# Kernel optimization log

Measured on AMD Instinct MI355X. Metric: run time of the kernel, lower is better.

## Reference

```python
import jax, jax.numpy as jnp
import numpy as np

B, C, M, H, W = 4, 12, 2, 320, 320
TOL = 1e-6
MAX_ITER = 10


def to_c(t):
    # [..., 2] real -> complex
    return jax.lax.complex(t[..., 0], t[..., 1])


def to_r(t):
    return jnp.stack([jnp.real(t), jnp.imag(t)], axis=-1)


def fft2c(x):
    return jnp.fft.fft2(x, axes=(-2, -1), norm='ortho')


def ifft2c(x):
    return jnp.fft.ifft2(x, axes=(-2, -1), norm='ortho')


def A_op(x, sm, mk):
    # x: [B,M,H,W] complex, sm: [B,C,M,H,W] complex, mk: [B,C,H,W] real
    coil_imgs = jnp.sum(x[:, None] * sm, axis=2)  # [B,C,H,W]
    return fft2c(coil_imgs) * mk


def AT_op(y, sm, mk):
    img = ifft2c(y * mk)  # [B,C,H,W]
    return jnp.sum(jnp.conj(sm) * img[:, :, None], axis=1)  # [B,M,H,W]


def cg_solve(x0, Mop, tol=TOL, max_iter=MAX_ITER):
    b = x0.shape[0]
    x0x0 = jnp.sum(jnp.abs(x0.reshape(b, -1)) ** 2, axis=-1)  # [B] real

    def body(carry, _):
        x, r, p, rr = carry
        active = jnp.min(rr / x0x0) > tol  # tol check, gated like the while-loop
        q = Mop(p)
        pq = jnp.sum((p * jnp.conj(q)).reshape(b, -1), axis=-1)  # complexDot(p, q)
        alpha = rr.astype(x0.dtype) / pq  # complex_div(rr, <p,q>)
        a = alpha[:, None, None, None]
        x_new = x + a * p
        r_new = r - a * q
        rr_new = jnp.sum(jnp.abs(r_new.reshape(b, -1)) ** 2, axis=-1)
        beta = (rr_new / rr)[:, None, None, None].astype(x0.dtype)
        p_new = r_new + beta * p
        new = (x_new, r_new, p_new, rr_new)
        carry = jax.tree.map(lambda n, o: jnp.where(active, n, o), new, carry)
        return carry, None

    rr0 = jnp.sum(jnp.abs(x0.reshape(b, -1)) ** 2, axis=-1)
    init = (jnp.zeros_like(x0), x0, x0, rr0)
    (x, _, _, _), _ = jax.lax.scan(body, init, None, length=max_iter)
    return x


def setup_inputs() -> dict:
    key = jax.random.key(0)
    k1, k2, k3, k4 = jax.random.split(key, 4)
    x = jax.random.normal(k1, (B, M, H, W, 2), dtype=jnp.float32)
    y = jax.random.normal(k2, (B, C, H, W, 2), dtype=jnp.float32)
    smaps = jax.random.normal(k3, (B, C, M, H, W, 2), dtype=jnp.float32) * 0.2
    mask = jax.random.randint(k4, (B, C, H, W, 1), 0, 2).astype(jnp.float32)
    lambda_a = jnp.full((1,), 0.05, dtype=jnp.float32)
    return {"x": x, "y": y, "smaps": smaps, "mask": mask, "lambda_a": lambda_a}


def reference(x, y, smaps, mask, lambda_a):
    z = to_c(x)          # [B,M,H,W]
    yc = to_c(y)         # [B,C,H,W]
    sm = to_c(smaps)     # [B,C,M,H,W]
    mk = mask[..., 0]    # [B,C,H,W]
    lam = lambda_a[0]

    x0 = lam * AT_op(yc, sm, mk) + z

    def Mop(p):
        return lam * AT_op(A_op(p, sm, mk), sm, mk) + p

    return to_r(cg_solve(x0, Mop))
```

## Files before the change

### kernel.cpp

```cpp
#include <hip/hip_runtime.h>
#include <math.h>

#define NB 4
#define NC 12
#define NM 2
#define NN 320
#define NHW (NN*NN)
#define NBC (NB*NC)
#define CG_TOL 1e-6f
#define NITER 10
#define PBLK 400
#define QBLK 320
#define QROW 4
#define LSTR (NN + 2)

#define TWO_PI_F 6.28318530717958647692f

typedef float2 c32;

__device__ __forceinline__ c32 cmul(c32 a, c32 b){ return make_float2(a.x*b.x - a.y*b.y, a.x*b.y + a.y*b.x); }
__device__ __forceinline__ c32 cmulj(c32 a, c32 b){ return make_float2(a.x*b.x + a.y*b.y, a.x*b.y - a.y*b.x); }
__device__ __forceinline__ c32 cadd(c32 a, c32 b){ return make_float2(a.x+b.x, a.y+b.y); }
__device__ __forceinline__ c32 csub(c32 a, c32 b){ return make_float2(a.x-b.x, a.y-b.y); }
__device__ __forceinline__ c32 cscale(c32 a, float s){ return make_float2(a.x*s, a.y*s); }

template<bool CONJ>
__device__ __forceinline__ c32 twmul(c32 a, c32 t){
  return CONJ ? make_float2(a.x*t.x + a.y*t.y, a.y*t.x - a.x*t.y)
              : make_float2(a.x*t.x - a.y*t.y, a.y*t.x + a.x*t.y);
}

__device__ __forceinline__ float wave_reduce_f(float v) {
  #pragma unroll
  for (int off = 32; off >= 1; off >>= 1) v += __shfl_xor(v, off, 64);
  return v;
}
__device__ __forceinline__ c32 wave_reduce_c(c32 v) {
  #pragma unroll
  for (int off = 32; off >= 1; off >>= 1) {
    v.x += __shfl_xor(v.x, off, 64);
    v.y += __shfl_xor(v.y, off, 64);
  }
  return v;
}

__global__ __launch_bounds__(256)
void twiddle_init(c32* __restrict__ T320, c32* __restrict__ T64)
{
  const int t = threadIdx.x;
  {
    float s, c; sincosf(TWO_PI_F * (float)t / 320.f, &s, &c);
    T320[t] = make_float2(c, s);
  }
  if (t < 32) {
    float s, c; sincosf(TWO_PI_F * (float)t / 64.f, &s, &c);
    T64[t] = make_float2(c, s);
  }
}

template<bool FWD>
__device__ __forceinline__ void radix5(c32 V[5]) {
  constexpr float C1 = 0.30901699437494745f;
  constexpr float S1 = 0.9510565162951535f;
  constexpr float C2 = -0.8090169943749475f;
  constexpr float S2 = 0.5877852522924731f;
  constexpr float sg = FWD ? -1.f : 1.f;
  const c32 w1 = make_float2(C1,  sg*S1);
  const c32 w2 = make_float2(C2,  sg*S2);
  const c32 w3 = make_float2(C2, -sg*S2);
  const c32 w4 = make_float2(C1, -sg*S1);
  c32 v0=V[0], v1=V[1], v2=V[2], v3=V[3], v4=V[4];
  V[0] = cadd(cadd(v0, v1), cadd(cadd(v2, v3), v4));
  V[1] = cadd(v0, cadd(cadd(cmul(v1,w1), cmul(v2,w2)), cadd(cmul(v3,w3), cmul(v4,w4))));
  V[2] = cadd(v0, cadd(cadd(cmul(v1,w2), cmul(v2,w4)), cadd(cmul(v3,w1), cmul(v4,w3))));
  V[3] = cadd(v0, cadd(cadd(cmul(v1,w3), cmul(v2,w1)), cadd(cmul(v3,w4), cmul(v4,w2))));
  V[4] = cadd(v0, cadd(cadd(cmul(v1,w4), cmul(v2,w3)), cadd(cmul(v3,w2), cmul(v4,w1))));
}

template<bool FWD>
__device__ __forceinline__ void fft320_x2(c32 A[5], c32 B[5],
                                          const c32 ct[4], const c32 tw[6], int lane)
{
  radix5<FWD>(A);
  radix5<FWD>(B);
  #pragma unroll
  for (int k = 1; k < 5; ++k) {
    A[k] = twmul<FWD>(A[k], ct[k-1]);
    B[k] = twmul<FWD>(B[k], ct[k-1]);
  }
  #pragma unroll
  for (int s = 0; s < 6; ++s) {
    const int m = 32 >> s;
    const c32 w = tw[s];
    const bool up = (lane & m) != 0;
    c32 oA[5], oB[5];
    #pragma unroll
    for (int k = 0; k < 5; ++k) { oA[k].x = __shfl_xor(A[k].x, m, 64); oA[k].y = __shfl_xor(A[k].y, m, 64); }
    #pragma unroll
    for (int k = 0; k < 5; ++k) { oB[k].x = __shfl_xor(B[k].x, m, 64); oB[k].y = __shfl_xor(B[k].y, m, 64); }
    #pragma unroll
    for (int k = 0; k < 5; ++k) {
      c32 loA = cadd(A[k], oA[k]);
      c32 hiA = twmul<FWD>(csub(oA[k], A[k]), w);
      A[k] = up ? hiA : loA;
      c32 loB = cadd(B[k], oB[k]);
      c32 hiB = twmul<FWD>(csub(oB[k], B[k]), w);
      B[k] = up ? hiB : loB;
    }
  }
}

template<bool FWD>
__device__ __forceinline__ void fft320_one(c32 A[5], const c32 ct[4], const c32 tw[6], int lane)
{
  radix5<FWD>(A);
  #pragma unroll
  for (int k = 1; k < 5; ++k) A[k] = twmul<FWD>(A[k], ct[k-1]);
  #pragma unroll
  for (int s = 0; s < 6; ++s) {
    const int m = 32 >> s;
    const c32 w = tw[s];
    const bool up = (lane & m) != 0;
    c32 o[5];
    #pragma unroll
    for (int k = 0; k < 5; ++k) { o[k].x = __shfl_xor(A[k].x, m, 64); o[k].y = __shfl_xor(A[k].y, m, 64); }
    #pragma unroll
    for (int k = 0; k < 5; ++k) {
      c32 lo = cadd(A[k], o[k]);
      c32 hi = twmul<FWD>(csub(o[k], A[k]), w);
      A[k] = up ? hi : lo;
    }
  }
}

#define LOAD_TWIDDLES \
  c32 ct[4], tw[6]; \
  _Pragma("unroll") for (int k_ = 0; k_ < 4; ++k_) ct[k_] = T320[(k_ + 1) * lane]; \
  _Pragma("unroll") for (int s_ = 0; s_ < 6; ++s_) tw[s_] = T64[(lane & ((32 >> s_) - 1)) << s_];

template<bool FWD, bool MASK_IN>
__global__ __launch_bounds__(256)
void fft_pass(const c32* __restrict__ in, c32* __restrict__ out,
              const float* __restrict__ mask,
              const c32* __restrict__ T320, const c32* __restrict__ T64)
{
  __shared__ c32 tile[8][LSTR];
  const int tid = threadIdx.x, lane = tid & 63, wv = tid >> 6;
  const int bc = blockIdx.y, r0 = blockIdx.x * 8;
  LOAD_TWIDDLES
  const int rv6 = __brev((unsigned)lane) >> 26;
  const int rA = r0 + wv*2, rB = rA + 1;
  c32 A[5], B[5];
  #pragma unroll
  for (int j = 0; j < 5; ++j) {
    const size_t iA = ((size_t)bc * NN + rA) * NN + lane + 64*j;
    const size_t iB = ((size_t)bc * NN + rB) * NN + lane + 64*j;
    A[j] = in[iA]; B[j] = in[iB];
    if constexpr (MASK_IN) { A[j] = cscale(A[j], mask[iA]); B[j] = cscale(B[j], mask[iB]); }
  }
  fft320_x2<FWD>(A, B, ct, tw, lane);
  #pragma unroll
  for (int k = 0; k < 5; ++k) {
    tile[wv*2    ][k + 5*rv6] = A[k];
    tile[wv*2 + 1][k + 5*rv6] = B[k];
  }
  __syncthreads();
  #pragma unroll
  for (int it = 0; it < 10; ++it) {
    const int idx = it * 256 + tid, u = idx >> 3, d = idx & 7;
    out[((size_t)bc * NN + u) * NN + (r0 + d)] = tile[d][u];
  }
}

__global__ __launch_bounds__(256)
void init_combine(const c32* __restrict__ img, const c32* __restrict__ smaps,
                  const c32* __restrict__ z, c32* __restrict__ x,
                  c32* __restrict__ r, c32* __restrict__ p,
                  const float* __restrict__ lam, float* __restrict__ part)
{
  const int b  = blockIdx.y;
  const int hw = blockIdx.x * 256 + threadIdx.x;
  const float l0 = lam[0] * (1.f / (float)NN);
  c32 a0 = make_float2(0.f,0.f), a1 = make_float2(0.f,0.f);
  #pragma unroll
  for (int c = 0; c < NC; ++c) {
    c32 iv = img[(size_t)(b*NC + c) * NHW + hw];
    c32 s0 = smaps[(size_t)((b*NC + c)*NM + 0) * NHW + hw];
    c32 s1 = smaps[(size_t)((b*NC + c)*NM + 1) * NHW + hw];
    a0 = cadd(a0, cmulj(s0, iv));
    a1 = cadd(a1, cmulj(s1, iv));
  }
  const size_t i0 = (size_t)(b*NM + 0) * NHW + hw;
  const size_t i1 = (size_t)(b*NM + 1) * NHW + hw;
  c32 x00 = cadd(cscale(a0, l0), z[i0]);
  c32 x01 = cadd(cscale(a1, l0), z[i1]);
  x[i0] = make_float2(0.f,0.f); x[i1] = make_float2(0.f,0.f);
  r[i0] = x00; r[i1] = x01;
  p[i0] = x00; p[i1] = x01;
  float acc = x00.x*x00.x + x00.y*x00.y + x01.x*x01.x + x01.y*x01.y;
  acc = wave_reduce_f(acc);
  __shared__ float sred[4];
  const int lane = threadIdx.x & 63, wv = threadIdx.x >> 6;
  if (lane == 0) sred[wv] = acc;
  __syncthreads();
  if (threadIdx.x == 0) part[b*PBLK + blockIdx.x] = sred[0]+sred[1]+sred[2]+sred[3];
}

__global__ __launch_bounds__(256)
void fft_comb(c32* __restrict__ out, const c32* __restrict__ pin,
              const c32* __restrict__ rres, c32* __restrict__ pout,
              const c32* __restrict__ smaps,
              float* __restrict__ rr, float* __restrict__ flags,
              const float* __restrict__ part1, const int it,
              const c32* __restrict__ T320, const c32* __restrict__ T64)
{
  __shared__ c32 tile[8][LSTR];
  __shared__ float sstat[NB];
  const int tid = threadIdx.x, lane = tid & 63, wv = tid >> 6;
  const int bc = blockIdx.y, r0 = blockIdx.x * 8;
  const int b = bc / NC, c = bc - b * NC;
  {
    float s = 0.f;
    for (int j = lane; j < PBLK; j += 64) s += part1[wv*PBLK + j];
    s = wave_reduce_f(s);
    if (lane == 0) sstat[wv] = s;
  }
  __syncthreads();
  float flag;
  if (it == 0) flag = 1.f;
  else {
    float mn = 1e30f;
    #pragma unroll
    for (int bb = 0; bb < NB; ++bb) mn = fminf(mn, sstat[bb] / rr[bb]);
    flag = (mn > CG_TOL) ? 1.f : 0.f;
  }
  if (tid < NB) rr[it*NB + tid] = sstat[tid];
  if (tid == 0) flags[it] = flag;
  if (it != 0 && flag == 0.f) return;
  const float beta = (it != 0) ? sstat[b] / rr[(it-1)*NB + b] : 0.f;
  const bool upd = (it != 0);

  LOAD_TWIDDLES
  const int rv6 = __brev((unsigned)lane) >> 26;
  const int rA = r0 + wv*2, rB = rA + 1;
  const size_t m0 = (size_t)(b*NM + 0) * NHW, m1 = (size_t)(b*NM + 1) * NHW;
  const size_t s0o = (size_t)((b*NC + c)*NM + 0) * NHW, s1o = (size_t)((b*NC + c)*NM + 1) * NHW;
  c32 A[5], B[5];
  #pragma unroll
  for (int j = 0; j < 5; ++j) {
    const size_t hA = (size_t)rA * NN + lane + 64*j;
    const size_t hB = (size_t)rB * NN + lane + 64*j;
    c32 r0A = rres[m0 + hA], r1A = rres[m1 + hA];
    c32 r0B = rres[m0 + hB], r1B = rres[m1 + hB];
    c32 p0A, p1A, p0B, p1B;
    if (upd) {
      p0A = cadd(r0A, cscale(pin[m0 + hA], beta));
      p1A = cadd(r1A, cscale(pin[m1 + hA], beta));
      p0B = cadd(r0B, cscale(pin[m0 + hB], beta));
      p1B = cadd(r1B, cscale(pin[m1 + hB], beta));
      if (c == 0) {
        pout[m0 + hA] = p0A; pout[m1 + hA] = p1A;
        pout[m0 + hB] = p0B; pout[m1 + hB] = p1B;
      }
    } else {
      p0A = r0A; p1A = r1A; p0B = r0B; p1B = r1B;
    }
    A[j] = cadd(cmul(p0A, smaps[s0o + hA]), cmul(p1A, smaps[s1o + hA]));
    B[j] = cadd(cmul(p0B, smaps[s0o + hB]), cmul(p1B, smaps[s1o + hB]));
  }
  fft320_x2<true>(A, B, ct, tw, lane);
  #pragma unroll
  for (int k = 0; k < 5; ++k) {
    tile[wv*2    ][k + 5*rv6] = A[k];
    tile[wv*2 + 1][k + 5*rv6] = B[k];
  }
  __syncthreads();
  #pragma unroll
  for (int it5 = 0; it5 < 10; ++it5) {
    const int idx = it5 * 256 + tid, u = idx >> 3, d = idx & 7;
    out[((size_t)bc * NN + u) * NN + (r0 + d)] = tile[d][u];
  }
}

__global__ __launch_bounds__(256)
void fft_mask_ifft(const c32* __restrict__ in, c32* __restrict__ out,
                   const float* __restrict__ mask, const float* __restrict__ flag,
                   const c32* __restrict__ T320, const c32* __restrict__ T64)
{
  if (flag[0] == 0.f) return;
  __shared__ c32 tile[8][LSTR];
  const int tid = threadIdx.x, lane = tid & 63, wv = tid >> 6;
  const int bc = blockIdx.y, r0 = blockIdx.x * 8;
  LOAD_TWIDDLES
  const int rv6 = __brev((unsigned)lane) >> 26;
  const int rA = r0 + wv*2, rB = rA + 1;
  c32 A[5], B[5];
  #pragma unroll
  for (int j = 0; j < 5; ++j) {
    A[j] = in[((size_t)bc * NN + rA) * NN + lane + 64*j];
    B[j] = in[((size_t)bc * NN + rB) * NN + lane + 64*j];
  }
  fft320_x2<true>(A, B, ct, tw, lane);
  #pragma unroll
  for (int k = 0; k < 5; ++k) {
    const int kh = k + 5*rv6;
    A[k] = cscale(A[k], mask[(size_t)bc * NHW + (size_t)kh * NN + rA]);
    B[k] = cscale(B[k], mask[(size_t)bc * NHW + (size_t)kh * NN + rB]);
  }
  #pragma unroll
  for (int k = 0; k < 5; ++k) {
    tile[wv*2    ][k + 5*rv6] = A[k];
    tile[wv*2 + 1][k + 5*rv6] = B[k];
  }
  #pragma unroll
  for (int j = 0; j < 5; ++j) {
    A[j] = tile[wv*2    ][lane + 64*j];
    B[j] = tile[wv*2 + 1][lane + 64*j];
  }
  fft320_x2<false>(A, B, ct, tw, lane);
  #pragma unroll
  for (int k = 0; k < 5; ++k) {
    tile[wv*2    ][k + 5*rv6] = A[k];
    tile[wv*2 + 1][k + 5*rv6] = B[k];
  }
  __syncthreads();
  #pragma unroll
  for (int it = 0; it < 10; ++it) {
    const int idx = it * 256 + tid, u = idx >> 3, d = idx & 7;
    out[((size_t)bc * NN + u) * NN + (r0 + d)] = tile[d][u];
  }
}

__global__ __launch_bounds__(256)
void ifft_q(const c32* __restrict__ bufin, const c32* __restrict__ smaps,
            const c32* __restrict__ p, c32* __restrict__ q,
            const float* __restrict__ lam, const float* __restrict__ flag,
            c32* __restrict__ pqpart,
            const c32* __restrict__ T320, const c32* __restrict__ T64)
{
  if (flag[0] == 0.f) return;
  __shared__ c32 tile[QROW][LSTR];
  const int tid = threadIdx.x, lane = tid & 63, wv = tid >> 6;
  const int b = blockIdx.y, h = blockIdx.x;
  LOAD_TWIDDLES
  const int rv6 = __brev((unsigned)lane) >> 26;
  const float lq = lam[0] * (1.f / (float)NHW);
  const size_t rowoff = (size_t)h * NN + lane;
  c32 acc0[5], acc1[5];
  #pragma unroll
  for (int j = 0; j < 5; ++j) { acc0[j] = make_float2(0.f,0.f); acc1[j] = make_float2(0.f,0.f); }

  for (int cc = 0; cc < 3; ++cc) {
    const int c = wv * 3 + cc;
    const size_t ib  = (size_t)(b*NC + c) * NHW + rowoff;
    const size_t is0 = (size_t)((b*NC + c)*NM + 0) * NHW + rowoff;
    const size_t is1 = (size_t)((b*NC + c)*NM + 1) * NHW + rowoff;
    c32 A[5], S0[5], S1[5];
    #pragma unroll
    for (int j = 0; j < 5; ++j) {
      A[j] = bufin[ib + 64*j]; S0[j] = smaps[is0 + 64*j]; S1[j] = smaps[is1 + 64*j];
    }
    fft320_one<false>(A, ct, tw, lane);
    #pragma unroll
    for (int k = 0; k < 5; ++k) tile[wv][k + 5*rv6] = A[k];
    #pragma unroll
    for (int j = 0; j < 5; ++j) {
      c32 v = tile[wv][lane + 64*j];
      acc0[j] = cadd(acc0[j], cmulj(S0[j], v));
      acc1[j] = cadd(acc1[j], cmulj(S1[j], v));
    }
  }
  c32* red = &tile[0][0];
  __syncthreads();
  if (wv >= 2) {
    const int base = (wv - 2) * 640;
    #pragma unroll
    for (int j = 0; j < 5; ++j) {
      red[base + j*64 + lane] = acc0[j];
      red[base + 320 + j*64 + lane] = acc1[j];
    }
  }
  __syncthreads();
  if (wv < 2) {
    const int base = wv * 640;
    #pragma unroll
    for (int j = 0; j < 5; ++j) {
      acc0[j] = cadd(acc0[j], red[base + j*64 + lane]);
      acc1[j] = cadd(acc1[j], red[base + 320 + j*64 + lane]);
    }
  }
  __syncthreads();
  if (wv == 1) {
    #pragma unroll
    for (int j = 0; j < 5; ++j) {
      red[j*64 + lane] = acc0[j];
      red[320 + j*64 + lane] = acc1[j];
    }
  }
  __syncthreads();
  if (wv == 0) {
    const size_t i0 = (size_t)(b*NM + 0) * NHW + rowoff;
    const size_t i1 = (size_t)(b*NM + 1) * NHW + rowoff;
    c32 pqs = make_float2(0.f, 0.f);
    #pragma unroll
    for (int j = 0; j < 5; ++j) {
      acc0[j] = cadd(acc0[j], red[j*64 + lane]);
      acc1[j] = cadd(acc1[j], red[320 + j*64 + lane]);
      c32 p0 = p[i0 + 64*j], p1 = p[i1 + 64*j];
      c32 q0 = cadd(cscale(acc0[j], lq), p0);
      c32 q1 = cadd(cscale(acc1[j], lq), p1);
      q[i0 + 64*j] = q0; q[i1 + 64*j] = q1;
      pqs = cadd(pqs, cadd(cmulj(q0, p0), cmulj(q1, p1)));
    }
    pqs = wave_reduce_c(pqs);
    if (lane == 0) pqpart[b*QBLK + h] = pqs;
  }
}

__global__ __launch_bounds__(256)
void update1(c32* __restrict__ x, c32* __restrict__ r,
             const c32* __restrict__ p, const c32* __restrict__ q,
             const float* __restrict__ rr, const c32* __restrict__ pqpart,
             const float* __restrict__ flag, float* __restrict__ part,
             const int it)
{
  if (flag[0] == 0.f) return;
  const int b = blockIdx.y;
  const int t = threadIdx.x;
  c32 s = make_float2(0.f, 0.f);
  for (int j = t; j < QBLK; j += 256) s = cadd(s, pqpart[b*QBLK + j]);
  s = wave_reduce_c(s);
  __shared__ c32 spq[4];
  const int lane = t & 63, wv = t >> 6;
  if (lane == 0) spq[wv] = s;
  __syncthreads();
  const c32 pqv = cadd(cadd(spq[0], spq[1]), cadd(spq[2], spq[3]));
  const float rrv = rr[it*NB + b];
  const float den = pqv.x*pqv.x + pqv.y*pqv.y;
  const c32 alpha = make_float2(rrv * pqv.x / den, -rrv * pqv.y / den);
  const int hw = blockIdx.x * 256 + t;
  float acc = 0.f;
  #pragma unroll
  for (int m = 0; m < NM; ++m) {
    const size_t idx = (size_t)(b*NM + m) * NHW + hw;
    c32 pe = p[idx], qe = q[idx];
    c32 xe = cadd(x[idx], cmul(alpha, pe));
    c32 re = csub(r[idx], cmul(alpha, qe));
    x[idx] = xe; r[idx] = re;
    acc += re.x*re.x + re.y*re.y;
  }
  acc = wave_reduce_f(acc);
  __shared__ float sred[4];
  if (lane == 0) sred[wv] = acc;
  __syncthreads();
  if (t == 0) part[b*PBLK + blockIdx.x] = sred[0]+sred[1]+sred[2]+sred[3];
}

extern "C" void kernel_launch(void* const* d_in, const int* in_sizes, int n_in,
                              void* d_out, int out_size, void* d_ws, size_t ws_size,
                              hipStream_t stream)
{
  const c32*  z   = (const c32*)d_in[0];
  const c32*  y   = (const c32*)d_in[1];
  const c32*  sm  = (const c32*)d_in[2];
  const float* mk = (const float*)d_in[3];
  const float* lam= (const float*)d_in[4];
  c32* x = (c32*)d_out;

  char* base = (char*)d_ws;
  size_t off = 0;
  auto walloc = [&](size_t bytes) -> void* {
    void* ptr = base + off;
    off += (bytes + 255) & ~(size_t)255;
    return ptr;
  };
  c32* buf1   = (c32*)walloc((size_t)NBC * NHW * sizeof(c32));
  c32* buf2   = (c32*)walloc((size_t)NBC * NHW * sizeof(c32));
  c32* rv     = (c32*)walloc((size_t)NB * NM * NHW * sizeof(c32));
  c32* pvA    = (c32*)walloc((size_t)NB * NM * NHW * sizeof(c32));
  c32* pvB    = (c32*)walloc((size_t)NB * NM * NHW * sizeof(c32));
  c32* qv     = (c32*)walloc((size_t)NB * NM * NHW * sizeof(c32));
  c32* pqpart = (c32*)walloc((size_t)NB * QBLK * sizeof(c32));
  float* rr   = (float*)walloc((NITER + 1) * NB * sizeof(float));
  float* flags= (float*)walloc((NITER + 1) * sizeof(float));
  float* part1= (float*)walloc((size_t)NB * PBLK * sizeof(float));
  c32* T320   = (c32*)walloc(256 * sizeof(c32));
  c32* T64    = (c32*)walloc(32 * sizeof(c32));
  (void)ws_size; (void)in_sizes; (void)n_in; (void)out_size;

  dim3 blk256(256);
  dim3 fgrid(NN / 8, NBC);
  dim3 qgrid(QBLK, NB);
  dim3 ugrid(PBLK, NB);

  twiddle_init<<<1, blk256, 0, stream>>>(T320, T64);

  fft_pass<false, true ><<<fgrid, blk256, 0, stream>>>(y,    buf2, mk,      T320, T64);
  fft_pass<false, false><<<fgrid, blk256, 0, stream>>>(buf2, buf1, nullptr, T320, T64);
  init_combine<<<ugrid, blk256, 0, stream>>>(buf1, sm, z, x, rv, pvA, lam, part1);

  for (int i = 0; i < NITER; ++i) {
    c32* pin  = (i & 1) ? pvA : pvB;
    c32* pout = (i & 1) ? pvB : pvA;
    fft_comb<<<fgrid, blk256, 0, stream>>>(buf2, pin, rv, pout, sm, rr, flags, part1, i, T320, T64);
    fft_mask_ifft<<<fgrid, blk256, 0, stream>>>(buf2, buf1, mk, flags + i, T320, T64);
    ifft_q<<<qgrid, blk256, 0, stream>>>(buf1, sm, pout, qv, lam, flags + i, pqpart, T320, T64);
    update1<<<ugrid, blk256, 0, stream>>>(x, rv, pout, qv, rr, pqpart, flags + i, part1, i);
  }
}
```

Baseline: 377.3 us.

## Split LDS tiles into planar real/imag arrays, swap FFT grid order, early-exit CG

Replaces the interleaved complex shared-memory tiles with separate real and imaginary float arrays padded to 328. The goal is to cut LDS bank conflicts in the bit-reversed stores and the transposed reads. The FFT grid now puts batch-coil on blockIdx.x and row groups on blockIdx.y, which changes how blocks are scheduled and how writes are spread across cache and memory channels. fft_comb also returns early once the previous iteration's flag is zero, skipping the partial-sum reduction after convergence, though with ten iterations and the test tolerance this path may rarely trigger.

```diff
diff --git a/kernel.cpp b/kernel.cpp
--- a/kernel.cpp
+++ b/kernel.cpp
@@ -11,8 +11,7 @@
 #define NITER 10
 #define PBLK 400
 #define QBLK 320
-#define QROW 4
-#define LSTR (NN + 2)
+#define LSTRF 328
 
 #define TWO_PI_F 6.28318530717958647692f
 
@@ -144,9 +143,9 @@
               const float* __restrict__ mask,
               const c32* __restrict__ T320, const c32* __restrict__ T64)
 {
-  __shared__ c32 tile[8][LSTR];
+  __shared__ float tX[8][LSTRF], tY[8][LSTRF];
   const int tid = threadIdx.x, lane = tid & 63, wv = tid >> 6;
-  const int bc = blockIdx.y, r0 = blockIdx.x * 8;
+  const int bc = blockIdx.x, r0 = blockIdx.y * 8;
   LOAD_TWIDDLES
   const int rv6 = __brev((unsigned)lane) >> 26;
   const int rA = r0 + wv*2, rB = rA + 1;
@@ -161,14 +160,15 @@
   fft320_x2<FWD>(A, B, ct, tw, lane);
   #pragma unroll
   for (int k = 0; k < 5; ++k) {
-    tile[wv*2    ][k + 5*rv6] = A[k];
-    tile[wv*2 + 1][k + 5*rv6] = B[k];
+    const int i = k + 5*rv6;
+    tX[wv*2    ][i] = A[k].x; tY[wv*2    ][i] = A[k].y;
+    tX[wv*2 + 1][i] = B[k].x; tY[wv*2 + 1][i] = B[k].y;
   }
   __syncthreads();
   #pragma unroll
   for (int it = 0; it < 10; ++it) {
     const int idx = it * 256 + tid, u = idx >> 3, d = idx & 7;
-    out[((size_t)bc * NN + u) * NN + (r0 + d)] = tile[d][u];
+    out[((size_t)bc * NN + u) * NN + (r0 + d)] = make_float2(tX[d][u], tY[d][u]);
   }
 }
 
@@ -214,11 +214,15 @@
               const float* __restrict__ part1, const int it,
               const c32* __restrict__ T320, const c32* __restrict__ T64)
 {
-  __shared__ c32 tile[8][LSTR];
+  __shared__ float tX[8][LSTRF], tY[8][LSTRF];
   __shared__ float sstat[NB];
   const int tid = threadIdx.x, lane = tid & 63, wv = tid >> 6;
-  const int bc = blockIdx.y, r0 = blockIdx.x * 8;
+  const int bc = blockIdx.x, r0 = blockIdx.y * 8;
   const int b = bc / NC, c = bc - b * NC;
+  if (it > 0 && flags[it-1] == 0.f) {
+    if (blockIdx.x == 0 && blockIdx.y == 0 && tid == 0) flags[it] = 0.f;
+    return;
+  }
   {
     float s = 0.f;
     for (int j = lane; j < PBLK; j += 64) s += part1[wv*PBLK + j];
@@ -271,14 +275,15 @@
   fft320_x2<true>(A, B, ct, tw, lane);
   #pragma unroll
   for (int k = 0; k < 5; ++k) {
-    tile[wv*2    ][k + 5*rv6] = A[k];
-    tile[wv*2 + 1][k + 5*rv6] = B[k];
+    const int i = k + 5*rv6;
+    tX[wv*2    ][i] = A[k].x; tY[wv*2    ][i] = A[k].y;
+    tX[wv*2 + 1][i] = B[k].x; tY[wv*2 + 1][i] = B[k].y;
   }
   __syncthreads();
   #pragma unroll
   for (int it5 = 0; it5 < 10; ++it5) {
     const int idx = it5 * 256 + tid, u = idx >> 3, d = idx & 7;
-    out[((size_t)bc * NN + u) * NN + (r0 + d)] = tile[d][u];
+    out[((size_t)bc * NN + u) * NN + (r0 + d)] = make_float2(tX[d][u], tY[d][u]);
   }
 }
 
@@ -288,9 +293,9 @@
                    const c32* __restrict__ T320, const c32* __restrict__ T64)
 {
   if (flag[0] == 0.f) return;
-  __shared__ c32 tile[8][LSTR];
+  __shared__ float tX[8][LSTRF], tY[8][LSTRF];
   const int tid = threadIdx.x, lane = tid & 63, wv = tid >> 6;
-  const int bc = blockIdx.y, r0 = blockIdx.x * 8;
+  const int bc = blockIdx.x, r0 = blockIdx.y * 8;
   LOAD_TWIDDLES
   const int rv6 = __brev((unsigned)lane) >> 26;
   const int rA = r0 + wv*2, rB = rA + 1;
@@ -309,25 +314,28 @@
   }
   #pragma unroll
   for (int k = 0; k < 5; ++k) {
-    tile[wv*2    ][k + 5*rv6] = A[k];
-    tile[wv*2 + 1][k + 5*rv6] = B[k];
+    const int i = k + 5*rv6;
+    tX[wv*2    ][i] = A[k].x; tY[wv*2    ][i] = A[k].y;
+    tX[wv*2 + 1][i] = B[k].x; tY[wv*2 + 1][i] = B[k].y;
   }
   #pragma unroll
   for (int j = 0; j < 5; ++j) {
-    A[j] = tile[wv*2    ][lane + 64*j];
-    B[j] = tile[wv*2 + 1][lane + 64*j];
+    const int i = lane + 64*j;
+    A[j] = make_float2(tX[wv*2][i], tY[wv*2][i]);
+    B[j] = make_float2(tX[wv*2 + 1][i], tY[wv*2 + 1][i]);
   }
   fft320_x2<false>(A, B, ct, tw, lane);
   #pragma unroll
   for (int k = 0; k < 5; ++k) {
-    tile[wv*2    ][k + 5*rv6] = A[k];
-    tile[wv*2 + 1][k + 5*rv6] = B[k];
+    const int i = k + 5*rv6;
+    tX[wv*2    ][i] = A[k].x; tY[wv*2    ][i] = A[k].y;
+    tX[wv*2 + 1][i] = B[k].x; tY[wv*2 + 1][i] = B[k].y;
   }
   __syncthreads();
   #pragma unroll
   for (int it = 0; it < 10; ++it) {
     const int idx = it * 256 + tid, u = idx >> 3, d = idx & 7;
-    out[((size_t)bc * NN + u) * NN + (r0 + d)] = tile[d][u];
+    out[((size_t)bc * NN + u) * NN + (r0 + d)] = make_float2(tX[d][u], tY[d][u]);
   }
 }
 
@@ -339,7 +347,7 @@
             const c32* __restrict__ T320, const c32* __restrict__ T64)
 {
   if (flag[0] == 0.f) return;
-  __shared__ c32 tile[QROW][LSTR];
+  __shared__ float tX[4][LSTRF], tY[4][LSTRF];
   const int tid = threadIdx.x, lane = tid & 63, wv = tid >> 6;
   const int b = blockIdx.y, h = blockIdx.x;
   LOAD_TWIDDLES
@@ -362,22 +370,27 @@
     }
     fft320_one<false>(A, ct, tw, lane);
     #pragma unroll
-    for (int k = 0; k < 5; ++k) tile[wv][k + 5*rv6] = A[k];
+    for (int k = 0; k < 5; ++k) {
+      const int i = k + 5*rv6;
+      tX[wv][i] = A[k].x; tY[wv][i] = A[k].y;
+    }
     #pragma unroll
     for (int j = 0; j < 5; ++j) {
-      c32 v = tile[wv][lane + 64*j];
+      const int i = lane + 64*j;
+      c32 v = make_float2(tX[wv][i], tY[wv][i]);
       acc0[j] = cadd(acc0[j], cmulj(S0[j], v));
       acc1[j] = cadd(acc1[j], cmulj(S1[j], v));
     }
   }
-  c32* red = &tile[0][0];
+  float* redX = &tX[0][0];
+  float* redY = &tY[0][0];
   __syncthreads();
   if (wv >= 2) {
     const int base = (wv - 2) * 640;
     #pragma unroll
     for (int j = 0; j < 5; ++j) {
-      red[base + j*64 + lane] = acc0[j];
-      red[base + 320 + j*64 + lane] = acc1[j];
+      redX[base + j*64 + lane] = acc0[j].x; redY[base + j*64 + lane] = acc0[j].y;
+      redX[base + 320 + j*64 + lane] = acc1[j].x; redY[base + 320 + j*64 + lane] = acc1[j].y;
     }
   }
   __syncthreads();
@@ -385,16 +398,16 @@
     const int base = wv * 640;
     #pragma unroll
     for (int j = 0; j < 5; ++j) {
-      acc0[j] = cadd(acc0[j], red[base + j*64 + lane]);
-      acc1[j] = cadd(acc1[j], red[base + 320 + j*64 + lane]);
+      acc0[j] = cadd(acc0[j], make_float2(redX[base + j*64 + lane], redY[base + j*64 + lane]));
+      acc1[j] = cadd(acc1[j], make_float2(redX[base + 320 + j*64 + lane], redY[base + 320 + j*64 + lane]));
     }
   }
   __syncthreads();
   if (wv == 1) {
     #pragma unroll
     for (int j = 0; j < 5; ++j) {
-      red[j*64 + lane] = acc0[j];
-      red[320 + j*64 + lane] = acc1[j];
+      redX[j*64 + lane] = acc0[j].x; redY[j*64 + lane] = acc0[j].y;
+      redX[320 + j*64 + lane] = acc1[j].x; redY[320 + j*64 + lane] = acc1[j].y;
     }
   }
   __syncthreads();
@@ -404,8 +417,8 @@
     c32 pqs = make_float2(0.f, 0.f);
     #pragma unroll
     for (int j = 0; j < 5; ++j) {
-      acc0[j] = cadd(acc0[j], red[j*64 + lane]);
-      acc1[j] = cadd(acc1[j], red[320 + j*64 + lane]);
+      acc0[j] = cadd(acc0[j], make_float2(redX[j*64 + lane], redY[j*64 + lane]));
+      acc1[j] = cadd(acc1[j], make_float2(redX[320 + j*64 + lane], redY[320 + j*64 + lane]));
       c32 p0 = p[i0 + 64*j], p1 = p[i1 + 64*j];
       c32 q0 = cadd(cscale(acc0[j], lq), p0);
       c32 q1 = cadd(cscale(acc1[j], lq), p1);
@@ -489,7 +502,7 @@
   (void)ws_size; (void)in_sizes; (void)n_in; (void)out_size;
 
   dim3 blk256(256);
-  dim3 fgrid(NN / 8, NBC);
+  dim3 fgrid(NBC, NN / 8);
   dim3 qgrid(QBLK, NB);
   dim3 ugrid(PBLK, NB);
 
```

After: 367.7 us. 2.5% less time.
